# Kernel optimization log

Measured on AMD Instinct MI355X. Metric: run time of the kernel, lower is better.

The kernel has to match this reference:

```python
import jax, jax.numpy as jnp
import numpy as np

EPS = 1e-6

def make_rotX(angs, eps=EPS):
    n = jnp.linalg.norm(angs, axis=-1) + eps
    c, s = angs[..., 0] / n, angs[..., 1] / n
    z = jnp.zeros_like(c); o = jnp.ones_like(c)
    return jnp.stack([
        jnp.stack([o, z, z, z], -1),
        jnp.stack([z, c, -s, z], -1),
        jnp.stack([z, s, c, z], -1),
        jnp.stack([z, z, z, o], -1)], -2)  # [B,L,4,4]

def make_rotZ(angs, eps=EPS):
    n = jnp.linalg.norm(angs, axis=-1) + eps
    c, s = angs[..., 0] / n, angs[..., 1] / n
    z = jnp.zeros_like(c); o = jnp.ones_like(c)
    return jnp.stack([
        jnp.stack([c, -s, z, z], -1),
        jnp.stack([s, c, z, z], -1),
        jnp.stack([z, z, o, z], -1),
        jnp.stack([z, z, z, o], -1)], -2)

def make_rot_axis(angs, u, eps=EPS):
    n = jnp.linalg.norm(angs, axis=-1) + eps
    ct, st = angs[..., 0] / n, angs[..., 1] / n
    u0, u1, u2 = u[..., 0], u[..., 1], u[..., 2]
    omc = 1.0 - ct
    z = jnp.zeros_like(ct); o = jnp.ones_like(ct)
    return jnp.stack([
        jnp.stack([ct + u0*u0*omc, u0*u1*omc - u2*st, u0*u2*omc + u1*st, z], -1),
        jnp.stack([u0*u1*omc + u2*st, ct + u1*u1*omc, u1*u2*omc - u0*st, z], -1),
        jnp.stack([u0*u2*omc - u1*st, u1*u2*omc + u0*st, ct + u2*u2*omc, z], -1),
        jnp.stack([z, z, z, o], -1)], -2)

def rigid_from_3_points(N, Ca, C, eps=1e-8):
    # Gram-Schmidt backbone frame (RF2 convention, non_ideal=False)
    v1 = C - Ca
    v2 = N - Ca
    e1 = v1 / (jnp.linalg.norm(v1, axis=-1, keepdims=True) + eps)
    u2 = v2 - jnp.sum(e1 * v2, -1, keepdims=True) * e1
    e2 = u2 / (jnp.linalg.norm(u2, axis=-1, keepdims=True) + eps)
    e3 = jnp.cross(e1, e2)
    R = jnp.stack([e1, e2, e3], axis=-1)  # columns e1,e2,e3
    return R, Ca


def setup_inputs() -> dict:
    key = jax.random.key(0)
    ks = jax.random.split(key, 6)
    B, L, NAA, NATOMS, NFRAMES = 1, 65536, 22, 27, 9
    xyz = jax.random.normal(ks[0], (B, L, 3, 3), dtype=jnp.float32)
    alphas = jax.random.normal(ks[1], (B, L, 10, 2), dtype=jnp.float32)
    RTs_in_base_frame = jax.random.normal(ks[2], (NAA, 7, 4, 4), dtype=jnp.float32)
    xyzs_in_base_frame = jax.random.normal(ks[3], (NAA, NATOMS, 4), dtype=jnp.float32)
    seq = jax.random.randint(ks[4], (B, L), 0, NAA)
    base_indices = jax.random.randint(ks[5], (NAA, NATOMS), 0, NFRAMES)
    return {"xyz": xyz, "alphas": alphas, "RTs_in_base_frame": RTs_in_base_frame,
            "xyzs_in_base_frame": xyzs_in_base_frame, "seq": seq, "base_indices": base_indices}


def reference(xyz, alphas, RTs_in_base_frame, xyzs_in_base_frame, seq, base_indices):
    B, L = xyz.shape[:2]
    dt = xyz.dtype
    Rs, Ts = rigid_from_3_points(xyz[..., 0, :], xyz[..., 1, :], xyz[..., 2, :])
    top = jnp.concatenate([Rs, Ts[..., None]], axis=-1)                    # [B,L,3,4]
    bottom = jnp.broadcast_to(jnp.array([0., 0., 0., 1.], dt), (B, L, 1, 4))
    RTF0 = jnp.concatenate([top, bottom], axis=-2)                         # [B,L,4,4]

    RT = RTs_in_base_frame[seq]        # [B,L,7,4,4]
    RTF1 = RTF0 @ RT[:, :, 0] @ make_rotX(alphas[:, :, 0])
    RTF2 = RTF0 @ RT[:, :, 1] @ make_rotX(alphas[:, :, 1])
    RTF3 = RTF0 @ RT[:, :, 2] @ make_rotX(alphas[:, :, 2])

    basexyzs = xyzs_in_base_frame[seq]  # [B,L,27,4]
    NCr = 0.5 * (basexyzs[:, :, 2, :3] + basexyzs[:, :, 0, :3])
    CAr = basexyzs[:, :, 1, :3]
    CBr = basexyzs[:, :, 4, :3]
    ax1 = jnp.cross(CBr - CAr, NCr - CAr)
    ax1 = ax1 / (jnp.linalg.norm(ax1, axis=-1, keepdims=True) + 1e-8)
    NCp = basexyzs[:, :, 2, :3] - basexyzs[:, :, 0, :3]
    NCpp = NCp - jnp.sum(NCp * NCr, -1, keepdims=True) / jnp.sum(NCr * NCr, -1, keepdims=True) * NCr
    ax2 = jnp.cross(CBr - CAr, NCpp)
    ax2 = ax2 / (jnp.linalg.norm(ax2, axis=-1, keepdims=True) + 1e-8)

    CBrot1 = make_rot_axis(alphas[:, :, 7], ax1)
    CBrot2 = make_rot_axis(alphas[:, :, 8], ax2)
    RTF8 = RTF0 @ CBrot1 @ CBrot2
    RTF4 = RTF8 @ RT[:, :, 3] @ make_rotX(alphas[:, :, 3]) @ make_rotZ(alphas[:, :, 9])
    RTF5 = RTF4 @ RT[:, :, 4] @ make_rotX(alphas[:, :, 4])
    RTF6 = RTF5 @ RT[:, :, 5] @ make_rotX(alphas[:, :, 5])
    RTF7 = RTF6 @ RT[:, :, 6] @ make_rotX(alphas[:, :, 6])

    RTframes = jnp.stack((RTF0, RTF1, RTF2, RTF3, RTF4, RTF5, RTF6, RTF7, RTF8), axis=2)  # [B,L,9,4,4]

    idx = base_indices[seq]  # [B,L,27] frame index per atom
    idxb = jnp.broadcast_to(idx[..., None, None], (B, L, idx.shape[2], 4, 4))
    frames = jnp.take_along_axis(RTframes, idxb, axis=2)  # [B,L,27,4,4]
    xyzs = jnp.einsum('blaij,blaj->blai', frames, basexyzs)
    return RTframes, xyzs[..., :3]
```

## Files before the change

### kernel.cpp

```cpp
#include <hip/hip_runtime.h>

#define TPB 128
#define FSTRIDE 108
#define NFRM 9
#define NATOMS 27


__device__ __forceinline__ void load16(float* M, const float* __restrict__ p) {
    const float4* q = reinterpret_cast<const float4*>(p);
    float4 v0 = q[0], v1 = q[1], v2 = q[2], v3 = q[3];
    M[0]=v0.x; M[1]=v0.y; M[2]=v0.z; M[3]=v0.w;
    M[4]=v1.x; M[5]=v1.y; M[6]=v1.z; M[7]=v1.w;
    M[8]=v2.x; M[9]=v2.y; M[10]=v2.z; M[11]=v2.w;
    M[12]=v3.x; M[13]=v3.y; M[14]=v3.z; M[15]=v3.w;
}

__device__ __forceinline__ void store16(float* __restrict__ p, const float* M) {
    float4* q = reinterpret_cast<float4*>(p);
    q[0] = make_float4(M[0],M[1],M[2],M[3]);
    q[1] = make_float4(M[4],M[5],M[6],M[7]);
    q[2] = make_float4(M[8],M[9],M[10],M[11]);
    q[3] = make_float4(M[12],M[13],M[14],M[15]);
}

__device__ __forceinline__ void stage12(float* sF, int tid, int f, const float* M) {
    float4* d = reinterpret_cast<float4*>(sF + tid*FSTRIDE + f*12);
    d[0] = make_float4(M[0],M[1],M[2],M[3]);
    d[1] = make_float4(M[4],M[5],M[6],M[7]);
    d[2] = make_float4(M[8],M[9],M[10],M[11]);
}

__device__ __forceinline__ void mul_affine(float* __restrict__ P,
                                           const float* __restrict__ Ar,
                                           const float* __restrict__ B) {
#pragma unroll
    for (int i = 0; i < 3; ++i) {
#pragma unroll
        for (int j = 0; j < 4; ++j) {
            float t = Ar[i*4+0] * B[0*4+j];
            t = fmaf(Ar[i*4+1], B[1*4+j], t);
            t = fmaf(Ar[i*4+2], B[2*4+j], t);
            t = fmaf(Ar[i*4+3], B[3*4+j], t);
            P[i*4+j] = t;
        }
    }
#pragma unroll
    for (int j = 0; j < 4; ++j) P[12+j] = B[12+j];
}

__device__ __forceinline__ void mul_full(float* __restrict__ P,
                                         const float* __restrict__ A,
                                         const float* __restrict__ B) {
#pragma unroll
    for (int i = 0; i < 4; ++i) {
#pragma unroll
        for (int j = 0; j < 4; ++j) {
            float t = A[i*4+0] * B[0*4+j];
            t = fmaf(A[i*4+1], B[1*4+j], t);
            t = fmaf(A[i*4+2], B[2*4+j], t);
            t = fmaf(A[i*4+3], B[3*4+j], t);
            P[i*4+j] = t;
        }
    }
}

__device__ __forceinline__ void apply_rotX(float* M, float c, float s) {
#pragma unroll
    for (int i = 0; i < 4; ++i) {
        float t1 = M[i*4+1], t2 = M[i*4+2];
        M[i*4+1] = fmaf(t2, s, t1*c);
        M[i*4+2] = fmaf(t2, c, -(t1*s));
    }
}

__device__ __forceinline__ void apply_rotZ(float* M, float c, float s) {
#pragma unroll
    for (int i = 0; i < 4; ++i) {
        float t0 = M[i*4+0], t1 = M[i*4+1];
        M[i*4+0] = fmaf(t1, s, t0*c);
        M[i*4+1] = fmaf(t1, c, -(t0*s));
    }
}

__device__ __forceinline__ void rot_axis3(float* R, float ct, float st,
                                          float u0, float u1, float u2) {
    float omc = 1.0f - ct;
    R[0] = ct + u0*u0*omc;       R[1] = u0*u1*omc - u2*st;   R[2] = u0*u2*omc + u1*st;
    R[3] = u0*u1*omc + u2*st;    R[4] = ct + u1*u1*omc;      R[5] = u1*u2*omc - u0*st;
    R[6] = u0*u2*omc - u1*st;    R[7] = u1*u2*omc + u0*st;   R[8] = ct + u2*u2*omc;
}

__device__ __forceinline__ void mul3_a4(float* C, const float* A, const float* B) {
#pragma unroll
    for (int i = 0; i < 3; ++i)
#pragma unroll
        for (int j = 0; j < 3; ++j) {
            float t = A[i*4+0] * B[0*3+j];
            t = fmaf(A[i*4+1], B[1*3+j], t);
            t = fmaf(A[i*4+2], B[2*3+j], t);
            C[i*3+j] = t;
        }
}

__device__ __forceinline__ void mul3(float* C, const float* A, const float* B) {
#pragma unroll
    for (int i = 0; i < 3; ++i)
#pragma unroll
        for (int j = 0; j < 3; ++j) {
            float t = A[i*3+0] * B[0*3+j];
            t = fmaf(A[i*3+1], B[1*3+j], t);
            t = fmaf(A[i*3+2], B[2*3+j], t);
            C[i*3+j] = t;
        }
}


extern "C" __global__ void __launch_bounds__(TPB, 1)
caac_kernel(const float* __restrict__ xyz,
            const float* __restrict__ alphas,
            const float* __restrict__ RTs,
            const float* __restrict__ bxyz,
            const int*   __restrict__ seq,
            const int*   __restrict__ bidx,
            float* __restrict__ outF,
            float* __restrict__ outX,
            int L)
{
    __shared__ float sF[TPB * FSTRIDE];
    __shared__ int   sSeq[TPB];

    const int tid = threadIdx.x;
    const int l   = blockIdx.x * TPB + tid;

    if (l < L) {
        const float* xp = xyz + (size_t)l * 9;
        float Nx=xp[0], Ny=xp[1], Nz=xp[2];
        float Ax=xp[3], Ay=xp[4], Az=xp[5];
        float Cx=xp[6], Cy=xp[7], Cz=xp[8];

        float v1x=Cx-Ax, v1y=Cy-Ay, v1z=Cz-Az;
        float v2x=Nx-Ax, v2y=Ny-Ay, v2z=Nz-Az;
        float n1 = sqrtf(v1x*v1x + v1y*v1y + v1z*v1z) + 1e-8f;
        float e1x=v1x/n1, e1y=v1y/n1, e1z=v1z/n1;
        float dp = e1x*v2x + e1y*v2y + e1z*v2z;
        float u2x = v2x - dp*e1x, u2y = v2y - dp*e1y, u2z = v2z - dp*e1z;
        float n2 = sqrtf(u2x*u2x + u2y*u2y + u2z*u2z) + 1e-8f;
        float e2x=u2x/n2, e2y=u2y/n2, e2z=u2z/n2;
        float e3x = e1y*e2z - e1z*e2y;
        float e3y = e1z*e2x - e1x*e2z;
        float e3z = e1x*e2y - e1y*e2x;

        float M0[12] = { e1x, e2x, e3x, Ax,
                         e1y, e2y, e3y, Ay,
                         e1z, e2z, e3z, Az };

        int s = seq[l];
        sSeq[tid] = s;

        float ca[10], sa[10];
        const float* ap = alphas + (size_t)l * 20;
#pragma unroll
        for (int k = 0; k < 10; ++k) {
            float a0 = ap[2*k], a1 = ap[2*k+1];
            float n = sqrtf(a0*a0 + a1*a1) + 1e-6f;
            ca[k] = a0 / n;
            sa[k] = a1 / n;
        }

        float* ofr = outF + (size_t)l * 144;

        {
            float F[16];
#pragma unroll
            for (int k = 0; k < 12; ++k) F[k] = M0[k];
            F[12]=0.f; F[13]=0.f; F[14]=0.f; F[15]=1.f;
            store16(ofr, F);
            stage12(sF, tid, 0, F);
        }

        const float* rtbase = RTs + (size_t)s * 112;

#pragma unroll
        for (int k = 0; k < 3; ++k) {
            float Bm[16]; load16(Bm, rtbase + k*16);
            float P[16];
            mul_affine(P, M0, Bm);
            apply_rotX(P, ca[k], sa[k]);
            store16(ofr + (k+1)*16, P);
            stage12(sF, tid, k+1, P);
        }

        const float* bx = bxyz + (size_t)s * 108;
        float4 b0 = ((const float4*)bx)[0];
        float4 b1 = ((const float4*)bx)[1];
        float4 b2 = ((const float4*)bx)[2];
        float4 b4 = ((const float4*)bx)[4];
        float NCrx = 0.5f*(b2.x+b0.x), NCry = 0.5f*(b2.y+b0.y), NCrz = 0.5f*(b2.z+b0.z);
        float CBAx = b4.x-b1.x, CBAy = b4.y-b1.y, CBAz = b4.z-b1.z;
        float NCAx = NCrx-b1.x, NCAy = NCry-b1.y, NCAz = NCrz-b1.z;
        float a1x = CBAy*NCAz - CBAz*NCAy;
        float a1y = CBAz*NCAx - CBAx*NCAz;
        float a1z = CBAx*NCAy - CBAy*NCAx;
        float a1n = sqrtf(a1x*a1x + a1y*a1y + a1z*a1z) + 1e-8f;
        a1x/=a1n; a1y/=a1n; a1z/=a1n;
        float NCpx = b2.x-b0.x, NCpy = b2.y-b0.y, NCpz = b2.z-b0.z;
        float num = NCpx*NCrx + NCpy*NCry + NCpz*NCrz;
        float den = NCrx*NCrx + NCry*NCry + NCrz*NCrz;
        float tq  = num / den;
        float NCppx = NCpx - tq*NCrx, NCppy = NCpy - tq*NCry, NCppz = NCpz - tq*NCrz;
        float a2x = CBAy*NCppz - CBAz*NCppy;
        float a2y = CBAz*NCppx - CBAx*NCppz;
        float a2z = CBAx*NCppy - CBAy*NCppx;
        float a2n = sqrtf(a2x*a2x + a2y*a2y + a2z*a2z) + 1e-8f;
        a2x/=a2n; a2y/=a2n; a2z/=a2n;

        float C1[9], C2[9], E[9], Fr[9];
        rot_axis3(C1, ca[7], sa[7], a1x, a1y, a1z);
        rot_axis3(C2, ca[8], sa[8], a2x, a2y, a2z);
        mul3_a4(E, M0, C1);
        mul3(Fr, E, C2);

        float M8[12] = { Fr[0],Fr[1],Fr[2],M0[3],
                         Fr[3],Fr[4],Fr[5],M0[7],
                         Fr[6],Fr[7],Fr[8],M0[11] };
        {
            float F[16];
#pragma unroll
            for (int k = 0; k < 12; ++k) F[k] = M8[k];
            F[12]=0.f; F[13]=0.f; F[14]=0.f; F[15]=1.f;
            store16(ofr + 8*16, F);
            stage12(sF, tid, 8, F);
        }

        float P[16];
        {
            float Bm[16]; load16(Bm, rtbase + 3*16);
            mul_affine(P, M8, Bm);
            apply_rotX(P, ca[3], sa[3]);
            apply_rotZ(P, ca[9], sa[9]);
            store16(ofr + 4*16, P);
            stage12(sF, tid, 4, P);
        }

#pragma unroll
        for (int k = 4; k < 7; ++k) {
            float Bm[16]; load16(Bm, rtbase + k*16);
            float Q[16];
            mul_full(Q, P, Bm);
            apply_rotX(Q, ca[k], sa[k]);
            store16(ofr + (k+1)*16, Q);
            stage12(sF, tid, k+1, Q);
#pragma unroll
            for (int z = 0; z < 16; ++z) P[z] = Q[z];
        }
    }

    __syncthreads();

    const int bb_res = blockIdx.x * TPB;
    int nres = L - bb_res; if (nres > TPB) nres = TPB;
    const unsigned total = (unsigned)nres * 81u;
    float* ox = outX + (size_t)bb_res * 81;
    for (unsigned i = tid; i < total; i += TPB) {
        unsigned r = i / 81u;
        unsigned c = i - r*81u;
        unsigned a = c / 3u;
        unsigned d = c - a*3u;
        int s2 = sSeq[r];
        int ii = s2*27 + (int)a;
        int idx = bidx[ii];
        float4 bv = ((const float4*)bxyz)[ii];
        const float4 fr = *((const float4*)(sF + r*FSTRIDE + idx*12 + d*4));
        float val = fr.x * bv.x;
        val = fmaf(fr.y, bv.y, val);
        val = fmaf(fr.z, bv.z, val);
        val = fmaf(fr.w, bv.w, val);
        ox[i] = val;
    }
}

extern "C" void kernel_launch(void* const* d_in, const int* in_sizes, int n_in,
                              void* d_out, int out_size, void* d_ws, size_t ws_size,
                              hipStream_t stream) {
    const float* xyz    = (const float*)d_in[0];
    const float* alphas = (const float*)d_in[1];
    const float* RTs    = (const float*)d_in[2];
    const float* bxyz   = (const float*)d_in[3];
    const int*   seq    = (const int*)d_in[4];
    const int*   bidx   = (const int*)d_in[5];
    const int L = in_sizes[4];
    float* outF = (float*)d_out;
    float* outX = outF + (size_t)L * 144;
    const int grid = (L + TPB - 1) / TPB;
    hipLaunchKernelGGL(caac_kernel, dim3(grid), dim3(TPB), 0, stream,
                       xyz, alphas, RTs, bxyz, seq, bidx, outF, outX, L);
}
```

Measured before the change: 102.4 us.

## Split fused kernel into frames and atoms kernels with shared-memory staged inputs

Splits the single fused kernel into two launches. The first computes the frames and writes them to global memory, loading xyz and alphas cooperatively into shared memory so the reads coalesce. The second gathers the frames back from global memory to compute atom coordinates with one thread per output element. This removes the large shared-memory frame staging that limited occupancy (launch_bounds 1), at the cost of an extra launch and of rereading the frames from global memory or L2.

```diff
diff --git a/kernel.cpp b/kernel.cpp
--- a/kernel.cpp
+++ b/kernel.cpp
@@ -1,9 +1,8 @@
 #include <hip/hip_runtime.h>
 
-#define TPB 128
-#define FSTRIDE 108
-#define NFRM 9
-#define NATOMS 27
+#define TPB1 128
+#define TPB2 256
+#define ASTRIDE 22
 
 
 __device__ __forceinline__ void load16(float* M, const float* __restrict__ p) {
@@ -23,13 +22,6 @@
     q[3] = make_float4(M[12],M[13],M[14],M[15]);
 }
 
-__device__ __forceinline__ void stage12(float* sF, int tid, int f, const float* M) {
-    float4* d = reinterpret_cast<float4*>(sF + tid*FSTRIDE + f*12);
-    d[0] = make_float4(M[0],M[1],M[2],M[3]);
-    d[1] = make_float4(M[4],M[5],M[6],M[7]);
-    d[2] = make_float4(M[8],M[9],M[10],M[11]);
-}
-
 __device__ __forceinline__ void mul_affine(float* __restrict__ P,
                                            const float* __restrict__ Ar,
                                            const float* __restrict__ B) {
@@ -115,168 +107,188 @@
 }
 
 
-extern "C" __global__ void __launch_bounds__(TPB, 1)
-caac_kernel(const float* __restrict__ xyz,
-            const float* __restrict__ alphas,
-            const float* __restrict__ RTs,
-            const float* __restrict__ bxyz,
-            const int*   __restrict__ seq,
-            const int*   __restrict__ bidx,
-            float* __restrict__ outF,
-            float* __restrict__ outX,
-            int L)
+extern "C" __global__ void __launch_bounds__(TPB1)
+frames_kernel(const float* __restrict__ xyz,
+              const float* __restrict__ alphas,
+              const float* __restrict__ RTs,
+              const float* __restrict__ bxyz,
+              const int*   __restrict__ seq,
+              float* __restrict__ outF,
+              int L)
 {
-    __shared__ float sF[TPB * FSTRIDE];
-    __shared__ int   sSeq[TPB];
-
-    const int tid = threadIdx.x;
-    const int l   = blockIdx.x * TPB + tid;
-
-    if (l < L) {
-        const float* xp = xyz + (size_t)l * 9;
-        float Nx=xp[0], Ny=xp[1], Nz=xp[2];
-        float Ax=xp[3], Ay=xp[4], Az=xp[5];
-        float Cx=xp[6], Cy=xp[7], Cz=xp[8];
-
-        float v1x=Cx-Ax, v1y=Cy-Ay, v1z=Cz-Az;
-        float v2x=Nx-Ax, v2y=Ny-Ay, v2z=Nz-Az;
-        float n1 = sqrtf(v1x*v1x + v1y*v1y + v1z*v1z) + 1e-8f;
-        float e1x=v1x/n1, e1y=v1y/n1, e1z=v1z/n1;
-        float dp = e1x*v2x + e1y*v2y + e1z*v2z;
-        float u2x = v2x - dp*e1x, u2y = v2y - dp*e1y, u2z = v2z - dp*e1z;
-        float n2 = sqrtf(u2x*u2x + u2y*u2y + u2z*u2z) + 1e-8f;
-        float e2x=u2x/n2, e2y=u2y/n2, e2z=u2z/n2;
-        float e3x = e1y*e2z - e1z*e2y;
-        float e3y = e1z*e2x - e1x*e2z;
-        float e3z = e1x*e2y - e1y*e2x;
-
-        float M0[12] = { e1x, e2x, e3x, Ax,
-                         e1y, e2y, e3y, Ay,
-                         e1z, e2z, e3z, Az };
-
-        int s = seq[l];
-        sSeq[tid] = s;
-
-        float ca[10], sa[10];
-        const float* ap = alphas + (size_t)l * 20;
-#pragma unroll
-        for (int k = 0; k < 10; ++k) {
-            float a0 = ap[2*k], a1 = ap[2*k+1];
-            float n = sqrtf(a0*a0 + a1*a1) + 1e-6f;
-            ca[k] = a0 / n;
-            sa[k] = a1 / n;
-        }
-
-        float* ofr = outF + (size_t)l * 144;
-
-        {
-            float F[16];
-#pragma unroll
-            for (int k = 0; k < 12; ++k) F[k] = M0[k];
-            F[12]=0.f; F[13]=0.f; F[14]=0.f; F[15]=1.f;
-            store16(ofr, F);
-            stage12(sF, tid, 0, F);
-        }
-
-        const float* rtbase = RTs + (size_t)s * 112;
-
-#pragma unroll
-        for (int k = 0; k < 3; ++k) {
-            float Bm[16]; load16(Bm, rtbase + k*16);
-            float P[16];
-            mul_affine(P, M0, Bm);
-            apply_rotX(P, ca[k], sa[k]);
-            store16(ofr + (k+1)*16, P);
-            stage12(sF, tid, k+1, P);
-        }
-
-        const float* bx = bxyz + (size_t)s * 108;
-        float4 b0 = ((const float4*)bx)[0];
-        float4 b1 = ((const float4*)bx)[1];
-        float4 b2 = ((const float4*)bx)[2];
-        float4 b4 = ((const float4*)bx)[4];
-        float NCrx = 0.5f*(b2.x+b0.x), NCry = 0.5f*(b2.y+b0.y), NCrz = 0.5f*(b2.z+b0.z);
-        float CBAx = b4.x-b1.x, CBAy = b4.y-b1.y, CBAz = b4.z-b1.z;
-        float NCAx = NCrx-b1.x, NCAy = NCry-b1.y, NCAz = NCrz-b1.z;
-        float a1x = CBAy*NCAz - CBAz*NCAy;
-        float a1y = CBAz*NCAx - CBAx*NCAz;
-        float a1z = CBAx*NCAy - CBAy*NCAx;
-        float a1n = sqrtf(a1x*a1x + a1y*a1y + a1z*a1z) + 1e-8f;
-        a1x/=a1n; a1y/=a1n; a1z/=a1n;
-        float NCpx = b2.x-b0.x, NCpy = b2.y-b0.y, NCpz = b2.z-b0.z;
-        float num = NCpx*NCrx + NCpy*NCry + NCpz*NCrz;
-        float den = NCrx*NCrx + NCry*NCry + NCrz*NCrz;
-        float tq  = num / den;
-        float NCppx = NCpx - tq*NCrx, NCppy = NCpy - tq*NCry, NCppz = NCpz - tq*NCrz;
-        float a2x = CBAy*NCppz - CBAz*NCppy;
-        float a2y = CBAz*NCppx - CBAx*NCppz;
-        float a2z = CBAx*NCppy - CBAy*NCppx;
-        float a2n = sqrtf(a2x*a2x + a2y*a2y + a2z*a2z) + 1e-8f;
-        a2x/=a2n; a2y/=a2n; a2z/=a2n;
-
-        float C1[9], C2[9], E[9], Fr[9];
-        rot_axis3(C1, ca[7], sa[7], a1x, a1y, a1z);
-        rot_axis3(C2, ca[8], sa[8], a2x, a2y, a2z);
-        mul3_a4(E, M0, C1);
-        mul3(Fr, E, C2);
-
-        float M8[12] = { Fr[0],Fr[1],Fr[2],M0[3],
-                         Fr[3],Fr[4],Fr[5],M0[7],
-                         Fr[6],Fr[7],Fr[8],M0[11] };
-        {
-            float F[16];
-#pragma unroll
-            for (int k = 0; k < 12; ++k) F[k] = M8[k];
-            F[12]=0.f; F[13]=0.f; F[14]=0.f; F[15]=1.f;
-            store16(ofr + 8*16, F);
-            stage12(sF, tid, 8, F);
-        }
-
+    __shared__ float sX[TPB1 * 9];
+    __shared__ float sA[TPB1 * ASTRIDE];
+
+    const int tid  = threadIdx.x;
+    const int base = blockIdx.x * TPB1;
+    const int l    = base + tid;
+
+    {
+        const float4* gx = reinterpret_cast<const float4*>(xyz + (size_t)base * 9);
+        int nfl4 = ((min(TPB1, L - base)) * 9) >> 2;
+        int nflt = min(TPB1, L - base) * 9;
+        for (int j = tid; j < nfl4; j += TPB1)
+            reinterpret_cast<float4*>(sX)[j] = gx[j];
+        for (int j = (nfl4 << 2) + tid; j < nflt; j += TPB1)
+            sX[j] = xyz[(size_t)base * 9 + j];
+
+        const float2* ga = reinterpret_cast<const float2*>(alphas + (size_t)base * 20);
+        int npairs = min(TPB1, L - base) * 10;
+        for (int j = tid; j < npairs; j += TPB1) {
+            int r = j / 10, o = j - r * 10;
+            reinterpret_cast<float2*>(sA + r * ASTRIDE)[o] = ga[j];
+        }
+    }
+    __syncthreads();
+
+    if (l >= L) return;
+
+    const float* xp = sX + tid * 9;
+    float Nx=xp[0], Ny=xp[1], Nz=xp[2];
+    float Ax=xp[3], Ay=xp[4], Az=xp[5];
+    float Cx=xp[6], Cy=xp[7], Cz=xp[8];
+
+    float v1x=Cx-Ax, v1y=Cy-Ay, v1z=Cz-Az;
+    float v2x=Nx-Ax, v2y=Ny-Ay, v2z=Nz-Az;
+    float n1 = sqrtf(v1x*v1x + v1y*v1y + v1z*v1z) + 1e-8f;
+    float e1x=v1x/n1, e1y=v1y/n1, e1z=v1z/n1;
+    float dp = e1x*v2x + e1y*v2y + e1z*v2z;
+    float u2x = v2x - dp*e1x, u2y = v2y - dp*e1y, u2z = v2z - dp*e1z;
+    float n2 = sqrtf(u2x*u2x + u2y*u2y + u2z*u2z) + 1e-8f;
+    float e2x=u2x/n2, e2y=u2y/n2, e2z=u2z/n2;
+    float e3x = e1y*e2z - e1z*e2y;
+    float e3y = e1z*e2x - e1x*e2z;
+    float e3z = e1x*e2y - e1y*e2x;
+
+    float M0[12] = { e1x, e2x, e3x, Ax,
+                     e1y, e2y, e3y, Ay,
+                     e1z, e2z, e3z, Az };
+
+    int s = seq[l];
+
+    float ca[10], sa[10];
+    const float* ap = sA + tid * ASTRIDE;
+#pragma unroll
+    for (int k = 0; k < 10; ++k) {
+        float a0 = ap[2*k], a1 = ap[2*k+1];
+        float n = sqrtf(a0*a0 + a1*a1) + 1e-6f;
+        ca[k] = a0 / n;
+        sa[k] = a1 / n;
+    }
+
+    float* ofr = outF + (size_t)l * 144;
+
+    {
+        float F[16];
+#pragma unroll
+        for (int k = 0; k < 12; ++k) F[k] = M0[k];
+        F[12]=0.f; F[13]=0.f; F[14]=0.f; F[15]=1.f;
+        store16(ofr, F);
+    }
+
+    const float* rtbase = RTs + (size_t)s * 112;
+
+#pragma unroll
+    for (int k = 0; k < 3; ++k) {
+        float Bm[16]; load16(Bm, rtbase + k*16);
         float P[16];
-        {
-            float Bm[16]; load16(Bm, rtbase + 3*16);
-            mul_affine(P, M8, Bm);
-            apply_rotX(P, ca[3], sa[3]);
-            apply_rotZ(P, ca[9], sa[9]);
-            store16(ofr + 4*16, P);
-            stage12(sF, tid, 4, P);
-        }
-
-#pragma unroll
-        for (int k = 4; k < 7; ++k) {
-            float Bm[16]; load16(Bm, rtbase + k*16);
-            float Q[16];
-            mul_full(Q, P, Bm);
-            apply_rotX(Q, ca[k], sa[k]);
-            store16(ofr + (k+1)*16, Q);
-            stage12(sF, tid, k+1, Q);
-#pragma unroll
-            for (int z = 0; z < 16; ++z) P[z] = Q[z];
-        }
-    }
-
-    __syncthreads();
-
-    const int bb_res = blockIdx.x * TPB;
-    int nres = L - bb_res; if (nres > TPB) nres = TPB;
-    const unsigned total = (unsigned)nres * 81u;
-    float* ox = outX + (size_t)bb_res * 81;
-    for (unsigned i = tid; i < total; i += TPB) {
-        unsigned r = i / 81u;
-        unsigned c = i - r*81u;
-        unsigned a = c / 3u;
-        unsigned d = c - a*3u;
-        int s2 = sSeq[r];
-        int ii = s2*27 + (int)a;
-        int idx = bidx[ii];
-        float4 bv = ((const float4*)bxyz)[ii];
-        const float4 fr = *((const float4*)(sF + r*FSTRIDE + idx*12 + d*4));
-        float val = fr.x * bv.x;
-        val = fmaf(fr.y, bv.y, val);
-        val = fmaf(fr.z, bv.z, val);
-        val = fmaf(fr.w, bv.w, val);
-        ox[i] = val;
-    }
+        mul_affine(P, M0, Bm);
+        apply_rotX(P, ca[k], sa[k]);
+        store16(ofr + (k+1)*16, P);
+    }
+
+    const float* bx = bxyz + (size_t)s * 108;
+    float4 b0 = ((const float4*)bx)[0];
+    float4 b1 = ((const float4*)bx)[1];
+    float4 b2 = ((const float4*)bx)[2];
+    float4 b4 = ((const float4*)bx)[4];
+    float NCrx = 0.5f*(b2.x+b0.x), NCry = 0.5f*(b2.y+b0.y), NCrz = 0.5f*(b2.z+b0.z);
+    float CBAx = b4.x-b1.x, CBAy = b4.y-b1.y, CBAz = b4.z-b1.z;
+    float NCAx = NCrx-b1.x, NCAy = NCry-b1.y, NCAz = NCrz-b1.z;
+    float a1x = CBAy*NCAz - CBAz*NCAy;
+    float a1y = CBAz*NCAx - CBAx*NCAz;
+    float a1z = CBAx*NCAy - CBAy*NCAx;
+    float a1n = sqrtf(a1x*a1x + a1y*a1y + a1z*a1z) + 1e-8f;
+    a1x/=a1n; a1y/=a1n; a1z/=a1n;
+    float NCpx = b2.x-b0.x, NCpy = b2.y-b0.y, NCpz = b2.z-b0.z;
+    float num = NCpx*NCrx + NCpy*NCry + NCpz*NCrz;
+    float den = NCrx*NCrx + NCry*NCry + NCrz*NCrz;
+    float tq  = num / den;
+    float NCppx = NCpx - tq*NCrx, NCppy = NCpy - tq*NCry, NCppz = NCpz - tq*NCrz;
+    float a2x = CBAy*NCppz - CBAz*NCppy;
+    float a2y = CBAz*NCppx - CBAx*NCppz;
+    float a2z = CBAx*NCppy - CBAy*NCppx;
+    float a2n = sqrtf(a2x*a2x + a2y*a2y + a2z*a2z) + 1e-8f;
+    a2x/=a2n; a2y/=a2n; a2z/=a2n;
+
+    float C1[9], C2[9], E[9], Fr[9];
+    rot_axis3(C1, ca[7], sa[7], a1x, a1y, a1z);
+    rot_axis3(C2, ca[8], sa[8], a2x, a2y, a2z);
+    mul3_a4(E, M0, C1);
+    mul3(Fr, E, C2);
+
+    float M8[12] = { Fr[0],Fr[1],Fr[2],M0[3],
+                     Fr[3],Fr[4],Fr[5],M0[7],
+                     Fr[6],Fr[7],Fr[8],M0[11] };
+    {
+        float F[16];
+#pragma unroll
+        for (int k = 0; k < 12; ++k) F[k] = M8[k];
+        F[12]=0.f; F[13]=0.f; F[14]=0.f; F[15]=1.f;
+        store16(ofr + 8*16, F);
+    }
+
+    float P[16];
+    {
+        float Bm[16]; load16(Bm, rtbase + 3*16);
+        mul_affine(P, M8, Bm);
+        apply_rotX(P, ca[3], sa[3]);
+        apply_rotZ(P, ca[9], sa[9]);
+        store16(ofr + 4*16, P);
+    }
+
+#pragma unroll
+    for (int k = 4; k < 7; ++k) {
+        float Bm[16]; load16(Bm, rtbase + k*16);
+        float Q[16];
+        mul_full(Q, P, Bm);
+        apply_rotX(Q, ca[k], sa[k]);
+        store16(ofr + (k+1)*16, Q);
+#pragma unroll
+        for (int z = 0; z < 16; ++z) P[z] = Q[z];
+    }
+}
+
+
+extern "C" __global__ void __launch_bounds__(TPB2)
+atoms_kernel(const float* __restrict__ outF,
+             const float* __restrict__ bxyz,
+             const int*   __restrict__ seq,
+             const int*   __restrict__ bidx,
+             float* __restrict__ outX,
+             int total)
+{
+    int i = blockIdx.x * TPB2 + threadIdx.x;
+    if (i >= total) return;
+
+    unsigned ui = (unsigned)i;
+    unsigned r = ui / 81u;
+    unsigned c = ui - r * 81u;
+    unsigned a = c / 3u;
+    unsigned d = c - a * 3u;
+
+    int s  = seq[r];
+    int ii = s * 27 + (int)a;
+    int idx = bidx[ii];
+
+    float4 bv = reinterpret_cast<const float4*>(bxyz)[ii];
+    float4 fr = *reinterpret_cast<const float4*>(outF + (size_t)r * 144 + idx * 16 + d * 4);
+
+    float val = fr.x * bv.x;
+    val = fmaf(fr.y, bv.y, val);
+    val = fmaf(fr.z, bv.z, val);
+    val = fmaf(fr.w, bv.w, val);
+    outX[i] = val;
 }
 
 extern "C" void kernel_launch(void* const* d_in, const int* in_sizes, int n_in,
@@ -291,7 +303,13 @@
     const int L = in_sizes[4];
     float* outF = (float*)d_out;
     float* outX = outF + (size_t)L * 144;
-    const int grid = (L + TPB - 1) / TPB;
-    hipLaunchKernelGGL(caac_kernel, dim3(grid), dim3(TPB), 0, stream,
-                       xyz, alphas, RTs, bxyz, seq, bidx, outF, outX, L);
-}
+
+    const int grid1 = (L + TPB1 - 1) / TPB1;
+    hipLaunchKernelGGL(frames_kernel, dim3(grid1), dim3(TPB1), 0, stream,
+                       xyz, alphas, RTs, bxyz, seq, outF, L);
+
+    const int total = L * 81;
+    const int grid2 = (total + TPB2 - 1) / TPB2;
+    hipLaunchKernelGGL(atoms_kernel, dim3(grid2), dim3(TPB2), 0, stream,
+                       outF, bxyz, seq, bidx, outX, total);
+}
```

Result: slower. 115.9 us (+13.2%).

## Split each residue's frame chain across four threads, one matrix row each

Applied to the files above, without the earlier changes.

Each residue is now handled by four threads, each computing one row of every frame matrix with vector-matrix products, instead of one thread computing full 4x4 products. Inputs (xyz, alphas, seq) are staged cooperatively into shared memory, and full frames are written to shared memory and then copied to global memory with coalesced float4 stores. The intent is to cut per-thread register pressure, raise occupancy, and make the frame output writes coalesced. In exchange, the 4th row's thread recomputes the chain redundantly, each thread reloads the RT matrices, and the block adds an extra barrier.

```diff
diff --git a/kernel.cpp b/kernel.cpp
--- a/kernel.cpp
+++ b/kernel.cpp
@@ -1,9 +1,8 @@
 #include <hip/hip_runtime.h>
 
-#define TPB 128
-#define FSTRIDE 108
-#define NFRM 9
-#define NATOMS 27
+#define TPB 256
+#define RPB 64
+#define ASTRIDE 21
 
 
 __device__ __forceinline__ void load16(float* M, const float* __restrict__ p) {
@@ -15,71 +14,29 @@
     M[12]=v3.x; M[13]=v3.y; M[14]=v3.z; M[15]=v3.w;
 }
 
-__device__ __forceinline__ void store16(float* __restrict__ p, const float* M) {
-    float4* q = reinterpret_cast<float4*>(p);
-    q[0] = make_float4(M[0],M[1],M[2],M[3]);
-    q[1] = make_float4(M[4],M[5],M[6],M[7]);
-    q[2] = make_float4(M[8],M[9],M[10],M[11]);
-    q[3] = make_float4(M[12],M[13],M[14],M[15]);
-}
-
-__device__ __forceinline__ void stage12(float* sF, int tid, int f, const float* M) {
-    float4* d = reinterpret_cast<float4*>(sF + tid*FSTRIDE + f*12);
-    d[0] = make_float4(M[0],M[1],M[2],M[3]);
-    d[1] = make_float4(M[4],M[5],M[6],M[7]);
-    d[2] = make_float4(M[8],M[9],M[10],M[11]);
-}
-
-__device__ __forceinline__ void mul_affine(float* __restrict__ P,
-                                           const float* __restrict__ Ar,
-                                           const float* __restrict__ B) {
-#pragma unroll
-    for (int i = 0; i < 3; ++i) {
-#pragma unroll
-        for (int j = 0; j < 4; ++j) {
-            float t = Ar[i*4+0] * B[0*4+j];
-            t = fmaf(Ar[i*4+1], B[1*4+j], t);
-            t = fmaf(Ar[i*4+2], B[2*4+j], t);
-            t = fmaf(Ar[i*4+3], B[3*4+j], t);
-            P[i*4+j] = t;
-        }
-    }
-#pragma unroll
-    for (int j = 0; j < 4; ++j) P[12+j] = B[12+j];
-}
-
-__device__ __forceinline__ void mul_full(float* __restrict__ P,
-                                         const float* __restrict__ A,
+__device__ __forceinline__ void vrow_mat(float* __restrict__ w,
+                                         const float* __restrict__ v,
                                          const float* __restrict__ B) {
 #pragma unroll
-    for (int i = 0; i < 4; ++i) {
-#pragma unroll
-        for (int j = 0; j < 4; ++j) {
-            float t = A[i*4+0] * B[0*4+j];
-            t = fmaf(A[i*4+1], B[1*4+j], t);
-            t = fmaf(A[i*4+2], B[2*4+j], t);
-            t = fmaf(A[i*4+3], B[3*4+j], t);
-            P[i*4+j] = t;
-        }
-    }
-}
-
-__device__ __forceinline__ void apply_rotX(float* M, float c, float s) {
-#pragma unroll
-    for (int i = 0; i < 4; ++i) {
-        float t1 = M[i*4+1], t2 = M[i*4+2];
-        M[i*4+1] = fmaf(t2, s, t1*c);
-        M[i*4+2] = fmaf(t2, c, -(t1*s));
-    }
-}
-
-__device__ __forceinline__ void apply_rotZ(float* M, float c, float s) {
-#pragma unroll
-    for (int i = 0; i < 4; ++i) {
-        float t0 = M[i*4+0], t1 = M[i*4+1];
-        M[i*4+0] = fmaf(t1, s, t0*c);
-        M[i*4+1] = fmaf(t1, c, -(t0*s));
-    }
+    for (int j = 0; j < 4; ++j) {
+        float t = v[0] * B[0*4+j];
+        t = fmaf(v[1], B[1*4+j], t);
+        t = fmaf(v[2], B[2*4+j], t);
+        t = fmaf(v[3], B[3*4+j], t);
+        w[j] = t;
+    }
+}
+
+__device__ __forceinline__ void vrotX(float* v, float c, float s) {
+    float t1 = v[1], t2 = v[2];
+    v[1] = fmaf(t2, s, t1*c);
+    v[2] = fmaf(t2, c, -(t1*s));
+}
+
+__device__ __forceinline__ void vrotZ(float* v, float c, float s) {
+    float t0 = v[0], t1 = v[1];
+    v[0] = fmaf(t1, s, t0*c);
+    v[1] = fmaf(t1, c, -(t0*s));
 }
 
 __device__ __forceinline__ void rot_axis3(float* R, float ct, float st,
@@ -90,32 +47,12 @@
     R[6] = u0*u2*omc - u1*st;    R[7] = u1*u2*omc + u0*st;   R[8] = ct + u2*u2*omc;
 }
 
-__device__ __forceinline__ void mul3_a4(float* C, const float* A, const float* B) {
-#pragma unroll
-    for (int i = 0; i < 3; ++i)
-#pragma unroll
-        for (int j = 0; j < 3; ++j) {
-            float t = A[i*4+0] * B[0*3+j];
-            t = fmaf(A[i*4+1], B[1*3+j], t);
-            t = fmaf(A[i*4+2], B[2*3+j], t);
-            C[i*3+j] = t;
-        }
-}
-
-__device__ __forceinline__ void mul3(float* C, const float* A, const float* B) {
-#pragma unroll
-    for (int i = 0; i < 3; ++i)
-#pragma unroll
-        for (int j = 0; j < 3; ++j) {
-            float t = A[i*3+0] * B[0*3+j];
-            t = fmaf(A[i*3+1], B[1*3+j], t);
-            t = fmaf(A[i*3+2], B[2*3+j], t);
-            C[i*3+j] = t;
-        }
-}
-
-
-extern "C" __global__ void __launch_bounds__(TPB, 1)
+__device__ __forceinline__ void st4(float* p, float a, float b, float c, float d) {
+    *reinterpret_cast<float4*>(p) = make_float4(a, b, c, d);
+}
+
+
+extern "C" __global__ void __launch_bounds__(TPB, 4)
 caac_kernel(const float* __restrict__ xyz,
             const float* __restrict__ alphas,
             const float* __restrict__ RTs,
@@ -126,39 +63,39 @@
             float* __restrict__ outX,
             int L)
 {
-    __shared__ float sF[TPB * FSTRIDE];
-    __shared__ int   sSeq[TPB];
-
-    const int tid = threadIdx.x;
-    const int l   = blockIdx.x * TPB + tid;
-
-    if (l < L) {
-        const float* xp = xyz + (size_t)l * 9;
-        float Nx=xp[0], Ny=xp[1], Nz=xp[2];
-        float Ax=xp[3], Ay=xp[4], Az=xp[5];
-        float Cx=xp[6], Cy=xp[7], Cz=xp[8];
-
-        float v1x=Cx-Ax, v1y=Cy-Ay, v1z=Cz-Az;
-        float v2x=Nx-Ax, v2y=Ny-Ay, v2z=Nz-Az;
-        float n1 = sqrtf(v1x*v1x + v1y*v1y + v1z*v1z) + 1e-8f;
-        float e1x=v1x/n1, e1y=v1y/n1, e1z=v1z/n1;
-        float dp = e1x*v2x + e1y*v2y + e1z*v2z;
-        float u2x = v2x - dp*e1x, u2y = v2y - dp*e1y, u2z = v2z - dp*e1z;
-        float n2 = sqrtf(u2x*u2x + u2y*u2y + u2z*u2z) + 1e-8f;
-        float e2x=u2x/n2, e2y=u2y/n2, e2z=u2z/n2;
-        float e3x = e1y*e2z - e1z*e2y;
-        float e3y = e1z*e2x - e1x*e2z;
-        float e3z = e1x*e2y - e1y*e2x;
-
-        float M0[12] = { e1x, e2x, e3x, Ax,
-                         e1y, e2y, e3y, Ay,
-                         e1z, e2z, e3z, Az };
-
-        int s = seq[l];
-        sSeq[tid] = s;
-
-        float ca[10], sa[10];
-        const float* ap = alphas + (size_t)l * 20;
+    __shared__ float sF[RPB * 144];
+    __shared__ int   sSeq[RPB];
+    float* sX = sF;
+    float* sA = sF + RPB * 9;
+
+    const int tid     = threadIdx.x;
+    const int row     = tid >> 6;
+    const int r       = tid & 63;
+    const int resBase = blockIdx.x * RPB;
+    int nres = L - resBase; if (nres > RPB) nres = RPB;
+
+    for (int j = tid; j < nres * 9; j += TPB)
+        sX[j] = xyz[(size_t)resBase * 9 + j];
+    for (int j = tid; j < nres * 20; j += TPB) {
+        int rr = j / 20, o = j - rr * 20;
+        sA[rr * ASTRIDE + o] = alphas[(size_t)resBase * 20 + j];
+    }
+    for (int j = tid; j < nres; j += TPB)
+        sSeq[j] = seq[resBase + j];
+    __syncthreads();
+
+    float ca[10], sa[10];
+    float v0[4] = {0.f, 0.f, 0.f, 1.f};
+    float v8[4] = {0.f, 0.f, 0.f, 1.f};
+    int s = 0;
+    float M0t = 0.f;
+
+    const bool active = (r < nres);
+    float e1x=0,e1y=0,e1z=0,e2x=0,e2y=0,e2z=0,e3x=0,e3y=0,e3z=0;
+
+    if (active) {
+        s = sSeq[r];
+        const float* ap = sA + r * ASTRIDE;
 #pragma unroll
         for (int k = 0; k < 10; ++k) {
             float a0 = ap[2*k], a1 = ap[2*k+1];
@@ -166,116 +103,136 @@
             ca[k] = a0 / n;
             sa[k] = a1 / n;
         }
-
-        float* ofr = outF + (size_t)l * 144;
-
-        {
-            float F[16];
-#pragma unroll
-            for (int k = 0; k < 12; ++k) F[k] = M0[k];
-            F[12]=0.f; F[13]=0.f; F[14]=0.f; F[15]=1.f;
-            store16(ofr, F);
-            stage12(sF, tid, 0, F);
-        }
-
+        if (row < 3) {
+            const float* xp = sX + r * 9;
+            float Nx=xp[0], Ny=xp[1], Nz=xp[2];
+            float Ax=xp[3], Ay=xp[4], Az=xp[5];
+            float Cx=xp[6], Cy=xp[7], Cz=xp[8];
+            float v1x=Cx-Ax, v1y=Cy-Ay, v1z=Cz-Az;
+            float v2x=Nx-Ax, v2y=Ny-Ay, v2z=Nz-Az;
+            float n1 = sqrtf(v1x*v1x + v1y*v1y + v1z*v1z) + 1e-8f;
+            e1x=v1x/n1; e1y=v1y/n1; e1z=v1z/n1;
+            float dp = e1x*v2x + e1y*v2y + e1z*v2z;
+            float u2x = v2x - dp*e1x, u2y = v2y - dp*e1y, u2z = v2z - dp*e1z;
+            float n2 = sqrtf(u2x*u2x + u2y*u2y + u2z*u2z) + 1e-8f;
+            e2x=u2x/n2; e2y=u2y/n2; e2z=u2z/n2;
+            e3x = e1y*e2z - e1z*e2y;
+            e3y = e1z*e2x - e1x*e2z;
+            e3z = e1x*e2y - e1y*e2x;
+            float Tr = (row == 0) ? Ax : (row == 1) ? Ay : Az;
+            v0[0] = (row == 0) ? e1x : (row == 1) ? e1y : e1z;
+            v0[1] = (row == 0) ? e2x : (row == 1) ? e2y : e2z;
+            v0[2] = (row == 0) ? e3x : (row == 1) ? e3y : e3z;
+            v0[3] = Tr;
+            M0t = Tr;
+        }
+    }
+    __syncthreads();
+
+    if (active) {
+        float* wf = sF + r * 144;
         const float* rtbase = RTs + (size_t)s * 112;
+
+        st4(wf + 0*16 + row*4, v0[0], v0[1], v0[2], v0[3]);
 
 #pragma unroll
         for (int k = 0; k < 3; ++k) {
             float Bm[16]; load16(Bm, rtbase + k*16);
-            float P[16];
-            mul_affine(P, M0, Bm);
-            apply_rotX(P, ca[k], sa[k]);
-            store16(ofr + (k+1)*16, P);
-            stage12(sF, tid, k+1, P);
-        }
-
-        const float* bx = bxyz + (size_t)s * 108;
-        float4 b0 = ((const float4*)bx)[0];
-        float4 b1 = ((const float4*)bx)[1];
-        float4 b2 = ((const float4*)bx)[2];
-        float4 b4 = ((const float4*)bx)[4];
-        float NCrx = 0.5f*(b2.x+b0.x), NCry = 0.5f*(b2.y+b0.y), NCrz = 0.5f*(b2.z+b0.z);
-        float CBAx = b4.x-b1.x, CBAy = b4.y-b1.y, CBAz = b4.z-b1.z;
-        float NCAx = NCrx-b1.x, NCAy = NCry-b1.y, NCAz = NCrz-b1.z;
-        float a1x = CBAy*NCAz - CBAz*NCAy;
-        float a1y = CBAz*NCAx - CBAx*NCAz;
-        float a1z = CBAx*NCAy - CBAy*NCAx;
-        float a1n = sqrtf(a1x*a1x + a1y*a1y + a1z*a1z) + 1e-8f;
-        a1x/=a1n; a1y/=a1n; a1z/=a1n;
-        float NCpx = b2.x-b0.x, NCpy = b2.y-b0.y, NCpz = b2.z-b0.z;
-        float num = NCpx*NCrx + NCpy*NCry + NCpz*NCrz;
-        float den = NCrx*NCrx + NCry*NCry + NCrz*NCrz;
-        float tq  = num / den;
-        float NCppx = NCpx - tq*NCrx, NCppy = NCpy - tq*NCry, NCppz = NCpz - tq*NCrz;
-        float a2x = CBAy*NCppz - CBAz*NCppy;
-        float a2y = CBAz*NCppx - CBAx*NCppz;
-        float a2z = CBAx*NCppy - CBAy*NCppx;
-        float a2n = sqrtf(a2x*a2x + a2y*a2y + a2z*a2z) + 1e-8f;
-        a2x/=a2n; a2y/=a2n; a2z/=a2n;
-
-        float C1[9], C2[9], E[9], Fr[9];
-        rot_axis3(C1, ca[7], sa[7], a1x, a1y, a1z);
-        rot_axis3(C2, ca[8], sa[8], a2x, a2y, a2z);
-        mul3_a4(E, M0, C1);
-        mul3(Fr, E, C2);
-
-        float M8[12] = { Fr[0],Fr[1],Fr[2],M0[3],
-                         Fr[3],Fr[4],Fr[5],M0[7],
-                         Fr[6],Fr[7],Fr[8],M0[11] };
-        {
-            float F[16];
-#pragma unroll
-            for (int k = 0; k < 12; ++k) F[k] = M8[k];
-            F[12]=0.f; F[13]=0.f; F[14]=0.f; F[15]=1.f;
-            store16(ofr + 8*16, F);
-            stage12(sF, tid, 8, F);
-        }
-
-        float P[16];
+            float w[4];
+            vrow_mat(w, v0, Bm);
+            vrotX(w, ca[k], sa[k]);
+            st4(wf + (k+1)*16 + row*4, w[0], w[1], w[2], w[3]);
+        }
+
+        if (row < 3) {
+            const float* bx = bxyz + (size_t)s * 108;
+            float4 b0 = ((const float4*)bx)[0];
+            float4 b1 = ((const float4*)bx)[1];
+            float4 b2 = ((const float4*)bx)[2];
+            float4 b4 = ((const float4*)bx)[4];
+            float NCrx = 0.5f*(b2.x+b0.x), NCry = 0.5f*(b2.y+b0.y), NCrz = 0.5f*(b2.z+b0.z);
+            float CBAx = b4.x-b1.x, CBAy = b4.y-b1.y, CBAz = b4.z-b1.z;
+            float NCAx = NCrx-b1.x, NCAy = NCry-b1.y, NCAz = NCrz-b1.z;
+            float a1x = CBAy*NCAz - CBAz*NCAy;
+            float a1y = CBAz*NCAx - CBAx*NCAz;
+            float a1z = CBAx*NCAy - CBAy*NCAx;
+            float a1n = sqrtf(a1x*a1x + a1y*a1y + a1z*a1z) + 1e-8f;
+            a1x/=a1n; a1y/=a1n; a1z/=a1n;
+            float NCpx = b2.x-b0.x, NCpy = b2.y-b0.y, NCpz = b2.z-b0.z;
+            float num = NCpx*NCrx + NCpy*NCry + NCpz*NCrz;
+            float den = NCrx*NCrx + NCry*NCry + NCrz*NCrz;
+            float tq  = num / den;
+            float NCppx = NCpx - tq*NCrx, NCppy = NCpy - tq*NCry, NCppz = NCpz - tq*NCrz;
+            float a2x = CBAy*NCppz - CBAz*NCppy;
+            float a2y = CBAz*NCppx - CBAx*NCppz;
+            float a2z = CBAx*NCppy - CBAy*NCppx;
+            float a2n = sqrtf(a2x*a2x + a2y*a2y + a2z*a2z) + 1e-8f;
+            a2x/=a2n; a2y/=a2n; a2z/=a2n;
+
+            float C1[9], C2[9];
+            rot_axis3(C1, ca[7], sa[7], a1x, a1y, a1z);
+            rot_axis3(C2, ca[8], sa[8], a2x, a2y, a2z);
+            float t0, t1, t2;
+            t0 = v0[0]*C1[0]; t0 = fmaf(v0[1], C1[3], t0); t0 = fmaf(v0[2], C1[6], t0);
+            t1 = v0[0]*C1[1]; t1 = fmaf(v0[1], C1[4], t1); t1 = fmaf(v0[2], C1[7], t1);
+            t2 = v0[0]*C1[2]; t2 = fmaf(v0[1], C1[5], t2); t2 = fmaf(v0[2], C1[8], t2);
+            float u0, u1, u2;
+            u0 = t0*C2[0]; u0 = fmaf(t1, C2[3], u0); u0 = fmaf(t2, C2[6], u0);
+            u1 = t0*C2[1]; u1 = fmaf(t1, C2[4], u1); u1 = fmaf(t2, C2[7], u1);
+            u2 = t0*C2[2]; u2 = fmaf(t1, C2[5], u2); u2 = fmaf(t2, C2[8], u2);
+            v8[0]=u0; v8[1]=u1; v8[2]=u2; v8[3]=M0t;
+        }
+        st4(wf + 8*16 + row*4, v8[0], v8[1], v8[2], v8[3]);
+
+        float p[4];
         {
             float Bm[16]; load16(Bm, rtbase + 3*16);
-            mul_affine(P, M8, Bm);
-            apply_rotX(P, ca[3], sa[3]);
-            apply_rotZ(P, ca[9], sa[9]);
-            store16(ofr + 4*16, P);
-            stage12(sF, tid, 4, P);
+            vrow_mat(p, v8, Bm);
+            vrotX(p, ca[3], sa[3]);
+            vrotZ(p, ca[9], sa[9]);
+            st4(wf + 4*16 + row*4, p[0], p[1], p[2], p[3]);
         }
 
 #pragma unroll
         for (int k = 4; k < 7; ++k) {
             float Bm[16]; load16(Bm, rtbase + k*16);
-            float Q[16];
-            mul_full(Q, P, Bm);
-            apply_rotX(Q, ca[k], sa[k]);
-            store16(ofr + (k+1)*16, Q);
-            stage12(sF, tid, k+1, Q);
-#pragma unroll
-            for (int z = 0; z < 16; ++z) P[z] = Q[z];
-        }
-    }
-
+            float q[4];
+            vrow_mat(q, p, Bm);
+            vrotX(q, ca[k], sa[k]);
+            st4(wf + (k+1)*16 + row*4, q[0], q[1], q[2], q[3]);
+            p[0]=q[0]; p[1]=q[1]; p[2]=q[2]; p[3]=q[3];
+        }
+    }
     __syncthreads();
 
-    const int bb_res = blockIdx.x * TPB;
-    int nres = L - bb_res; if (nres > TPB) nres = TPB;
-    const unsigned total = (unsigned)nres * 81u;
-    float* ox = outX + (size_t)bb_res * 81;
-    for (unsigned i = tid; i < total; i += TPB) {
-        unsigned r = i / 81u;
-        unsigned c = i - r*81u;
-        unsigned a = c / 3u;
-        unsigned d = c - a*3u;
-        int s2 = sSeq[r];
-        int ii = s2*27 + (int)a;
-        int idx = bidx[ii];
-        float4 bv = ((const float4*)bxyz)[ii];
-        const float4 fr = *((const float4*)(sF + r*FSTRIDE + idx*12 + d*4));
-        float val = fr.x * bv.x;
-        val = fmaf(fr.y, bv.y, val);
-        val = fmaf(fr.z, bv.z, val);
-        val = fmaf(fr.w, bv.w, val);
-        ox[i] = val;
+    {
+        const int n4 = nres * 36;
+        float4* dst = reinterpret_cast<float4*>(outF + (size_t)resBase * 144);
+        const float4* src = reinterpret_cast<const float4*>(sF);
+        for (int j = tid; j < n4; j += TPB)
+            dst[j] = src[j];
+    }
+
+    {
+        const int total = nres * 81;
+        float* ox = outX + (size_t)resBase * 81;
+        for (int i = tid; i < total; i += TPB) {
+            unsigned ui = (unsigned)i;
+            unsigned r2 = ui / 81u;
+            unsigned c  = ui - r2 * 81u;
+            unsigned a  = c / 3u;
+            unsigned d  = c - a * 3u;
+            int s2  = sSeq[r2];
+            int ii  = s2 * 27 + (int)a;
+            int idx = bidx[ii];
+            float4 bv = reinterpret_cast<const float4*>(bxyz)[ii];
+            float4 fr = *reinterpret_cast<const float4*>(sF + r2*144 + idx*16 + d*4);
+            float val = fr.x * bv.x;
+            val = fmaf(fr.y, bv.y, val);
+            val = fmaf(fr.z, bv.z, val);
+            val = fmaf(fr.w, bv.w, val);
+            ox[i] = val;
+        }
     }
 }
 
@@ -291,7 +248,8 @@
     const int L = in_sizes[4];
     float* outF = (float*)d_out;
     float* outX = outF + (size_t)L * 144;
-    const int grid = (L + TPB - 1) / TPB;
+
+    const int grid = (L + RPB - 1) / RPB;
     hipLaunchKernelGGL(caac_kernel, dim3(grid), dim3(TPB), 0, stream,
                        xyz, alphas, RTs, bxyz, seq, bidx, outF, outX, L);
 }
```

New measurement: 99.14 us. 1.03x faster.
